# Kernel tuning notes

Measured on AMD Instinct MI355X. Metric: run time of the kernel, lower is better.

## Reference

```python
import jax, jax.numpy as jnp
import numpy as np

MUL = 128          # multiplicity for every irrep
N = 100000         # number of nodes
INV_SQRT_FANIN = 1.0 / np.sqrt(MUL).astype(np.float32)


def setup_inputs() -> dict:
    key = jax.random.key(0)
    k = jax.random.split(key, 5)
    return {
        "x": jax.random.normal(k[0], (N, MUL + 3 * MUL), dtype=jnp.float32),   # [N, 512] = 128x0e + 128x1o
        "w1_s": jax.random.normal(k[1], (MUL, 2 * MUL), dtype=jnp.float32),    # 0e path of linear_1 (-> scalars+gates)
        "w1_v": jax.random.normal(k[2], (MUL, MUL), dtype=jnp.float32),        # 1o path of linear_1
        "w2_s": jax.random.normal(k[3], (MUL, MUL), dtype=jnp.float32),        # 0e path of linear_2
        "w2_v": jax.random.normal(k[4], (MUL, MUL), dtype=jnp.float32),        # 1o path of linear_2
    }


def reference(x, w1_s, w1_v, w2_s, w2_v):
    n = x.shape[0]
    x0 = x[:, :MUL]                              # [N, 128]  scalars (0e)
    x1 = x[:, MUL:].reshape(n, MUL, 3)           # [N, 128, 3] vectors (1o)

    # linear_1: 128x0e+128x1o -> 256x0e + 128x1o (scalars | gates | gated)
    s = (x0 @ w1_s) * INV_SQRT_FANIN             # [N, 256]
    v = jnp.einsum('nui,uv->nvi', x1, w1_v) * INV_SQRT_FANIN  # [N, 128, 3]

    # Gate: silu on scalars, silu(gates) broadcast-multiplies the vectors
    h0 = jax.nn.silu(s[:, :MUL])                 # [N, 128]
    g = jax.nn.silu(s[:, MUL:])                  # [N, 128]
    h1 = v * g[:, :, None]                       # [N, 128, 3]

    # linear_2: 128x0e+128x1o -> 128x0e+128x1o
    y0 = (h0 @ w2_s) * INV_SQRT_FANIN            # [N, 128]
    y1 = jnp.einsum('nui,uv->nvi', h1, w2_v) * INV_SQRT_FANIN  # [N, 128, 3]
    return jnp.concatenate([y0, y1.reshape(n, 3 * MUL)], axis=-1)  # [N, 512]
```

## Files before the change

### kernel.cpp

```cpp
#include <hip/hip_runtime.h>
#include <cstdint>

#define TPB  512
#define ROWS 32

typedef __attribute__((ext_vector_type(8))) short  short8;
typedef __attribute__((ext_vector_type(8))) __bf16 bf16x8;
typedef __attribute__((ext_vector_type(4))) float  f32x4;
typedef __attribute__((ext_vector_type(4))) short  short4v;

__device__ __forceinline__ short f2bf(float f) {
    union { float f; unsigned int u; } v; v.f = f;
    unsigned int u = v.u;
    u += 0x7fffu + ((u >> 16) & 1u);
    return (short)(u >> 16);
}
__device__ __forceinline__ float silu_f(float x) { return x / (1.0f + __expf(-x)); }

#define RSB 256
#define OFF_H0 32768
#define SMEM_BYTES 40960

__device__ __forceinline__ int swz(int row, int b) { return row * RSB + (b ^ ((row & 7) << 4)); }

__device__ __forceinline__ short8 lds_bfrag(const char* base, int off, int r0, int ks, int lane) {
    int row = r0 + (lane & 15);
    int bi  = ks * 64 + ((lane >> 4) << 4);
    return *(const short8*)(base + off + swz(row, bi));
}

template<bool PACKED>
__device__ __forceinline__ short8 wfrag(const short8* pw, const float* W, int ldn,
                                        int gtile, int ltile, int ks, int lane) {
    if constexpr (PACKED) {
        return pw[(gtile * 4 + ks) * 64 + lane];
    } else {
        const float* p = W + (size_t)(ks * 32 + ((lane >> 4) << 3)) * ldn + ltile * 16 + (lane & 15);
        short8 r;
#pragma unroll
        for (int j = 0; j < 8; ++j) r[j] = f2bf(p[(size_t)j * ldn]);
        return r;
    }
}

__device__ __forceinline__ f32x4 mfma16(short8 a, short8 b, f32x4 c) {
    return __builtin_amdgcn_mfma_f32_16x16x32_bf16(
        __builtin_bit_cast(bf16x8, a), __builtin_bit_cast(bf16x8, b), c, 0, 0, 0);
}

__global__ void prep_pack(const float* __restrict__ w1s, const float* __restrict__ w1v,
                          const float* __restrict__ w2s, const float* __restrict__ w2v,
                          short8* __restrict__ pk) {
    int b = blockIdx.x, t = threadIdx.x;
    int ks = t >> 6, lane = t & 63;
    const float* W; int ldn, lt;
    if (b < 16)      { W = w1s; ldn = 256; lt = b; }
    else if (b < 24) { W = w1v; ldn = 128; lt = b - 16; }
    else if (b < 32) { W = w2s; ldn = 128; lt = b - 24; }
    else             { W = w2v; ldn = 128; lt = b - 32; }
    const float* p = W + (size_t)(ks * 32 + ((lane >> 4) << 3)) * ldn + lt * 16 + (lane & 15);
    short8 r;
#pragma unroll
    for (int j = 0; j < 8; ++j) r[j] = f2bf(p[(size_t)j * ldn]);
    pk[(b * 4 + ks) * 64 + lane] = r;
}

template<bool PACKED>
__global__ __launch_bounds__(TPB, 4) void gnlr_fused_kernel(
    const float* __restrict__ x,
    const float* __restrict__ w1s, const float* __restrict__ w1v,
    const float* __restrict__ w2s, const float* __restrict__ w2v,
    const short8* __restrict__ pw,
    float* __restrict__ out, int n)
{
    __shared__ alignas(16) char sm[SMEM_BYTES];

    const int tid   = threadIdx.x;
    const int lane  = tid & 63;
    const int w     = tid >> 6;
    const int c0    = w * 16;
    const float INV = 0.08838834764831845f;
    const f32x4 z = { 0.f, 0.f, 0.f, 0.f };

    const int ntile = n >> 5;
    const int t0 = blockIdx.x * 2;
    const int t1 = t0 + 1;
    const bool has1 = (t1 < ntile);

    float4 st[8];

    auto issue = [&](int tile) {
        const float* xb = x + (size_t)tile * ROWS * 512;
#pragma unroll
        for (int it = 0; it < 2; ++it) {
            int idx = tid + it * TPB;
            int row = idx >> 5, c4 = (idx & 31) << 2;
            st[it] = *(const float4*)(xb + row * 512 + c4);
        }
#pragma unroll
        for (int it = 0; it < 2; ++it) {
            int idx = tid + it * TPB;
            int row = idx >> 5, grp = idx & 31;
            const float* p = xb + row * 512 + 128 + grp * 12;
            st[2 + it * 3 + 0] = *(const float4*)(p);
            st[2 + it * 3 + 1] = *(const float4*)(p + 4);
            st[2 + it * 3 + 2] = *(const float4*)(p + 8);
        }
    };

    auto writeLDS = [&]() {
#pragma unroll
        for (int it = 0; it < 2; ++it) {
            int idx = tid + it * TPB;
            int row = idx >> 5, c4 = (idx & 31) << 2;
            float4 f = st[it];
            short4v pk;
            pk.x = f2bf(f.x); pk.y = f2bf(f.y); pk.z = f2bf(f.z); pk.w = f2bf(f.w);
            *(short4v*)(sm + swz(row, c4 * 2)) = pk;
        }
#pragma unroll
        for (int it = 0; it < 2; ++it) {
            int idx = tid + it * TPB;
            int row = idx >> 5, grp = idx & 31;
            float4 fa = st[2 + it * 3 + 0], fb = st[2 + it * 3 + 1], fc = st[2 + it * 3 + 2];
            float fv[12] = { fa.x, fa.y, fa.z, fa.w, fb.x, fb.y, fb.z, fb.w, fc.x, fc.y, fc.z, fc.w };
#pragma unroll
            for (int i = 0; i < 3; ++i) {
                short4v pk;
                pk.x = f2bf(fv[i]); pk.y = f2bf(fv[3 + i]); pk.z = f2bf(fv[6 + i]); pk.w = f2bf(fv[9 + i]);
                *(short4v*)(sm + 8192 + i * 8192 + swz(row, grp * 8)) = pk;
            }
        }
    };

    auto computeTile = [&](int tile) {
        const int row0g = tile * ROWS;

        float g_reg[2][4];
        {
            short8 bs[4];
#pragma unroll
            for (int ks = 0; ks < 4; ++ks) bs[ks] = wfrag<PACKED>(pw, w1s, 256, w, w, ks, lane);
#pragma unroll
            for (int rt = 0; rt < 2; ++rt) {
                f32x4 acc = z;
#pragma unroll
                for (int ks = 0; ks < 4; ++ks)
                    acc = mfma16(bs[ks], lds_bfrag(sm, 0, rt * 16, ks, lane), acc);
                short4v pkv;
#pragma unroll
                for (int j = 0; j < 4; ++j) pkv[j] = f2bf(silu_f(acc[j] * INV));
                int row = rt * 16 + (lane & 15);
                *(short4v*)(sm + OFF_H0 + swz(row, 2 * (c0 + ((lane >> 4) << 2)))) = pkv;
            }
#pragma unroll
            for (int ks = 0; ks < 4; ++ks) bs[ks] = wfrag<PACKED>(pw, w1s, 256, 8 + w, 8 + w, ks, lane);
#pragma unroll
            for (int rt = 0; rt < 2; ++rt) {
                f32x4 acc = z;
#pragma unroll
                for (int ks = 0; ks < 4; ++ks)
                    acc = mfma16(bs[ks], lds_bfrag(sm, 0, rt * 16, ks, lane), acc);
#pragma unroll
                for (int j = 0; j < 4; ++j) g_reg[rt][j] = silu_f(acc[j] * INV);
            }
        }

        {
            short8 bv[4];
#pragma unroll
            for (int ks = 0; ks < 4; ++ks) bv[ks] = wfrag<PACKED>(pw, w1v, 128, 16 + w, w, ks, lane);
#pragma unroll
            for (int i = 0; i < 3; ++i) {
                __syncthreads();
#pragma unroll
                for (int rt = 0; rt < 2; ++rt) {
                    f32x4 acc = z;
#pragma unroll
                    for (int ks = 0; ks < 4; ++ks)
                        acc = mfma16(bv[ks], lds_bfrag(sm, 8192 + i * 8192, rt * 16, ks, lane), acc);
                    short4v pkv;
#pragma unroll
                    for (int j = 0; j < 4; ++j) pkv[j] = f2bf(acc[j] * INV * g_reg[rt][j]);
                    int row = rt * 16 + (lane & 15);
                    *(short4v*)(sm + i * 8192 + swz(row, 2 * (c0 + ((lane >> 4) << 2)))) = pkv;
                }
            }
        }
        __syncthreads();

        {
            short8 b2[4];
#pragma unroll
            for (int ks = 0; ks < 4; ++ks) b2[ks] = wfrag<PACKED>(pw, w2s, 128, 24 + w, w, ks, lane);
#pragma unroll
            for (int rt = 0; rt < 2; ++rt) {
                f32x4 acc = z;
#pragma unroll
                for (int ks = 0; ks < 4; ++ks)
                    acc = mfma16(b2[ks], lds_bfrag(sm, OFF_H0, rt * 16, ks, lane), acc);
                int rg = row0g + rt * 16 + (lane & 15);
                if (rg < n) {
                    float4 o = { acc[0] * INV, acc[1] * INV, acc[2] * INV, acc[3] * INV };
                    *(float4*)(out + (size_t)rg * 512 + c0 + ((lane >> 4) << 2)) = o;
                }
            }
#pragma unroll
            for (int ks = 0; ks < 4; ++ks) b2[ks] = wfrag<PACKED>(pw, w2v, 128, 32 + w, w, ks, lane);
#pragma unroll
            for (int rt = 0; rt < 2; ++rt) {
                f32x4 a3[3];
#pragma unroll
                for (int i = 0; i < 3; ++i) {
                    a3[i] = z;
#pragma unroll
                    for (int ks = 0; ks < 4; ++ks)
                        a3[i] = mfma16(b2[ks], lds_bfrag(sm, i * 8192, rt * 16, ks, lane), a3[i]);
                }
                int rg = row0g + rt * 16 + (lane & 15);
                if (rg < n) {
                    float* base = out + (size_t)rg * 512 + 128 + 3 * (c0 + ((lane >> 4) << 2));
                    float4 s0 = { a3[0][0] * INV, a3[1][0] * INV, a3[2][0] * INV, a3[0][1] * INV };
                    float4 s1 = { a3[1][1] * INV, a3[2][1] * INV, a3[0][2] * INV, a3[1][2] * INV };
                    float4 s2 = { a3[2][2] * INV, a3[0][3] * INV, a3[1][3] * INV, a3[2][3] * INV };
                    *(float4*)(base + 0) = s0;
                    *(float4*)(base + 4) = s1;
                    *(float4*)(base + 8) = s2;
                }
            }
        }
    };

    issue(t0);
    writeLDS();
    __syncthreads();
    if (has1) issue(t1);
    computeTile(t0);
    if (has1) {
        __syncthreads();
        writeLDS();
        __syncthreads();
        computeTile(t1);
    }
}

extern "C" void kernel_launch(void* const* d_in, const int* in_sizes, int n_in,
                              void* d_out, int out_size, void* d_ws, size_t ws_size,
                              hipStream_t stream) {
    const float* x   = (const float*)d_in[0];
    const float* w1s = (const float*)d_in[1];
    const float* w1v = (const float*)d_in[2];
    const float* w2s = (const float*)d_in[3];
    const float* w2v = (const float*)d_in[4];
    float* out = (float*)d_out;
    const int n = in_sizes[0] / 512;
    const int ntile = n / ROWS;
    const int grid = (ntile + 1) / 2;
    const size_t need = (size_t)40 * 4 * 64 * sizeof(short8);
    if (ws_size >= need) {
        prep_pack<<<40, 256, 0, stream>>>(w1s, w1v, w2s, w2v, (short8*)d_ws);
        gnlr_fused_kernel<true><<<grid, TPB, 0, stream>>>(x, w1s, w1v, w2s, w2v,
                                                          (const short8*)d_ws, out, n);
    } else {
        gnlr_fused_kernel<false><<<grid, TPB, 0, stream>>>(x, w1s, w1v, w2s, w2v,
                                                           nullptr, out, n);
    }
}
```

Baseline: 122.1 us.

## Convert to persistent grid-stride loop with register-held intermediates

Replaces the two-tiles-per-block launch with a persistent grid of fixed size that loops over tiles with a stride equal to the grid, prefetching the next tile's global loads into registers during compute. Intermediate h0/h1 results are kept in registers and written to LDS only after one barrier, which removes the three per-component barriers and the separate h0 LDS region. The aim is to cut launch and tail overhead and barrier stalls. In exchange it raises register pressure and drops the row bounds checks, which is only safe when n is a multiple of 32, and the fixed grid may not match the CU count well.

```diff
diff --git a/kernel.cpp b/kernel.cpp
--- a/kernel.cpp
+++ b/kernel.cpp
@@ -3,6 +3,7 @@
 
 #define TPB  512
 #define ROWS 32
+#define GRID 768
 
 typedef __attribute__((ext_vector_type(8))) short  short8;
 typedef __attribute__((ext_vector_type(8))) __bf16 bf16x8;
@@ -18,7 +19,6 @@
 __device__ __forceinline__ float silu_f(float x) { return x / (1.0f + __expf(-x)); }
 
 #define RSB 256
-#define OFF_H0 32768
 #define SMEM_BYTES 40960
 
 __device__ __forceinline__ int swz(int row, int b) { return row * RSB + (b ^ ((row & 7) << 4)); }
@@ -81,11 +81,7 @@
     const int c0    = w * 16;
     const float INV = 0.08838834764831845f;
     const f32x4 z = { 0.f, 0.f, 0.f, 0.f };
-
     const int ntile = n >> 5;
-    const int t0 = blockIdx.x * 2;
-    const int t1 = t0 + 1;
-    const bool has1 = (t1 < ntile);
 
     float4 st[8];
 
@@ -133,10 +129,19 @@
         }
     };
 
-    auto computeTile = [&](int tile) {
-        const int row0g = tile * ROWS;
-
-        float g_reg[2][4];
+    int t = blockIdx.x;
+    if (t >= ntile) return;
+    issue(t);
+    writeLDS();
+    __syncthreads();
+
+    while (true) {
+        int tn = t + GRID;
+        bool has = (tn < ntile);
+        if (has) issue(tn);
+
+        short4v h0pk[2];
+        float   g_reg[2][4];
         {
             short8 bs[4];
 #pragma unroll
@@ -147,11 +152,8 @@
 #pragma unroll
                 for (int ks = 0; ks < 4; ++ks)
                     acc = mfma16(bs[ks], lds_bfrag(sm, 0, rt * 16, ks, lane), acc);
-                short4v pkv;
-#pragma unroll
-                for (int j = 0; j < 4; ++j) pkv[j] = f2bf(silu_f(acc[j] * INV));
-                int row = rt * 16 + (lane & 15);
-                *(short4v*)(sm + OFF_H0 + swz(row, 2 * (c0 + ((lane >> 4) << 2)))) = pkv;
+#pragma unroll
+                for (int j = 0; j < 4; ++j) h0pk[rt][j] = f2bf(silu_f(acc[j] * INV));
             }
 #pragma unroll
             for (int ks = 0; ks < 4; ++ks) bs[ks] = wfrag<PACKED>(pw, w1s, 256, 8 + w, 8 + w, ks, lane);
@@ -166,30 +168,39 @@
             }
         }
 
+        short4v h1pk[3][2];
         {
             short8 bv[4];
 #pragma unroll
             for (int ks = 0; ks < 4; ++ks) bv[ks] = wfrag<PACKED>(pw, w1v, 128, 16 + w, w, ks, lane);
 #pragma unroll
             for (int i = 0; i < 3; ++i) {
-                __syncthreads();
 #pragma unroll
                 for (int rt = 0; rt < 2; ++rt) {
                     f32x4 acc = z;
 #pragma unroll
                     for (int ks = 0; ks < 4; ++ks)
                         acc = mfma16(bv[ks], lds_bfrag(sm, 8192 + i * 8192, rt * 16, ks, lane), acc);
-                    short4v pkv;
-#pragma unroll
-                    for (int j = 0; j < 4; ++j) pkv[j] = f2bf(acc[j] * INV * g_reg[rt][j]);
-                    int row = rt * 16 + (lane & 15);
-                    *(short4v*)(sm + i * 8192 + swz(row, 2 * (c0 + ((lane >> 4) << 2)))) = pkv;
+#pragma unroll
+                    for (int j = 0; j < 4; ++j) h1pk[i][rt][j] = f2bf(acc[j] * INV * g_reg[rt][j]);
                 }
             }
         }
         __syncthreads();
 
+#pragma unroll
+        for (int rt = 0; rt < 2; ++rt) {
+            int row = rt * 16 + (lane & 15);
+            int bi  = 2 * (c0 + ((lane >> 4) << 2));
+            *(short4v*)(sm + swz(row, bi)) = h0pk[rt];
+#pragma unroll
+            for (int i = 0; i < 3; ++i)
+                *(short4v*)(sm + 8192 + i * 8192 + swz(row, bi)) = h1pk[i][rt];
+        }
+        __syncthreads();
+
         {
+            const int row0g = t * ROWS;
             short8 b2[4];
 #pragma unroll
             for (int ks = 0; ks < 4; ++ks) b2[ks] = wfrag<PACKED>(pw, w2s, 128, 24 + w, w, ks, lane);
@@ -198,12 +209,10 @@
                 f32x4 acc = z;
 #pragma unroll
                 for (int ks = 0; ks < 4; ++ks)
-                    acc = mfma16(b2[ks], lds_bfrag(sm, OFF_H0, rt * 16, ks, lane), acc);
+                    acc = mfma16(b2[ks], lds_bfrag(sm, 0, rt * 16, ks, lane), acc);
                 int rg = row0g + rt * 16 + (lane & 15);
-                if (rg < n) {
-                    float4 o = { acc[0] * INV, acc[1] * INV, acc[2] * INV, acc[3] * INV };
-                    *(float4*)(out + (size_t)rg * 512 + c0 + ((lane >> 4) << 2)) = o;
-                }
+                float4 o = { acc[0] * INV, acc[1] * INV, acc[2] * INV, acc[3] * INV };
+                *(float4*)(out + (size_t)rg * 512 + c0 + ((lane >> 4) << 2)) = o;
             }
 #pragma unroll
             for (int ks = 0; ks < 4; ++ks) b2[ks] = wfrag<PACKED>(pw, w2v, 128, 32 + w, w, ks, lane);
@@ -215,32 +224,24 @@
                     a3[i] = z;
 #pragma unroll
                     for (int ks = 0; ks < 4; ++ks)
-                        a3[i] = mfma16(b2[ks], lds_bfrag(sm, i * 8192, rt * 16, ks, lane), a3[i]);
+                        a3[i] = mfma16(b2[ks], lds_bfrag(sm, 8192 + i * 8192, rt * 16, ks, lane), a3[i]);
                 }
                 int rg = row0g + rt * 16 + (lane & 15);
-                if (rg < n) {
-                    float* base = out + (size_t)rg * 512 + 128 + 3 * (c0 + ((lane >> 4) << 2));
-                    float4 s0 = { a3[0][0] * INV, a3[1][0] * INV, a3[2][0] * INV, a3[0][1] * INV };
-                    float4 s1 = { a3[1][1] * INV, a3[2][1] * INV, a3[0][2] * INV, a3[1][2] * INV };
-                    float4 s2 = { a3[2][2] * INV, a3[0][3] * INV, a3[1][3] * INV, a3[2][3] * INV };
-                    *(float4*)(base + 0) = s0;
-                    *(float4*)(base + 4) = s1;
-                    *(float4*)(base + 8) = s2;
-                }
-            }
-        }
-    };
-
-    issue(t0);
-    writeLDS();
-    __syncthreads();
-    if (has1) issue(t1);
-    computeTile(t0);
-    if (has1) {
+                float* base = out + (size_t)rg * 512 + 128 + 3 * (c0 + ((lane >> 4) << 2));
+                float4 s0 = { a3[0][0] * INV, a3[1][0] * INV, a3[2][0] * INV, a3[0][1] * INV };
+                float4 s1 = { a3[1][1] * INV, a3[2][1] * INV, a3[0][2] * INV, a3[1][2] * INV };
+                float4 s2 = { a3[2][2] * INV, a3[0][3] * INV, a3[1][3] * INV, a3[2][3] * INV };
+                *(float4*)(base + 0) = s0;
+                *(float4*)(base + 4) = s1;
+                *(float4*)(base + 8) = s2;
+            }
+        }
+
+        if (!has) break;
         __syncthreads();
         writeLDS();
         __syncthreads();
-        computeTile(t1);
+        t = tn;
     }
 }
 
@@ -254,15 +255,13 @@
     const float* w2v = (const float*)d_in[4];
     float* out = (float*)d_out;
     const int n = in_sizes[0] / 512;
-    const int ntile = n / ROWS;
-    const int grid = (ntile + 1) / 2;
     const size_t need = (size_t)40 * 4 * 64 * sizeof(short8);
     if (ws_size >= need) {
         prep_pack<<<40, 256, 0, stream>>>(w1s, w1v, w2s, w2v, (short8*)d_ws);
-        gnlr_fused_kernel<true><<<grid, TPB, 0, stream>>>(x, w1s, w1v, w2s, w2v,
+        gnlr_fused_kernel<true><<<GRID, TPB, 0, stream>>>(x, w1s, w1v, w2s, w2v,
                                                           (const short8*)d_ws, out, n);
     } else {
-        gnlr_fused_kernel<false><<<grid, TPB, 0, stream>>>(x, w1s, w1v, w2s, w2v,
+        gnlr_fused_kernel<false><<<GRID, TPB, 0, stream>>>(x, w1s, w1v, w2s, w2v,
                                                            nullptr, out, n);
     }
 }
```

New measurement: 226.2 us. 85.2% more time.
